# Kernel tuning notes

Hardware: AMD Instinct MI355X
Metric: run time of the kernel (lower is better)

The kernel has to match this reference:

```python
import jax, jax.numpy as jnp
import numpy as np

EPS = 1e-7  # tf.keras.backend.epsilon()
NUM_ROUTING = 3


def squash(v, axis=-1):
    s2 = jnp.sum(jnp.square(v), axis=axis, keepdims=True)
    scale = s2 / (1.0 + s2)
    return scale * v / jnp.sqrt(s2 + EPS)


def setup_inputs() -> dict:
    key = jax.random.key(0)
    kx, kw = jax.random.split(key)
    B, IN_CAPS, IN_DIM = 64, 2048, 16
    NUM_CAPS, OUT_DIM = 32, 16  # OUT_DIM must equal IN_DIM per the tf.matmul in call()
    x = jax.random.normal(kx, (B, IN_CAPS, IN_DIM), dtype=jnp.float32)
    # glorot_uniform over [in_caps, num_caps, in_dim, out_dim]
    limit = float(np.sqrt(6.0 / (IN_DIM + OUT_DIM)))
    W = jax.random.uniform(kw, (IN_CAPS, NUM_CAPS, IN_DIM, OUT_DIM),
                           minval=-limit, maxval=limit, dtype=jnp.float32)
    return {"x": x, "W": W}


def reference(x, W):
    # u_hat[b,i,j,d] = sum_k W[i,j,d,k] * x[b,i,k]   (tf.matmul(W, x[...,None]))
    u_hat = jnp.einsum('ijdk,bik->bijd', W, x)  # [B, in_caps, num_caps, dim]
    b = jnp.zeros(u_hat.shape[:-1], dtype=u_hat.dtype)  # [B, in_caps, num_caps]
    outputs = None
    for i in range(NUM_ROUTING):
        c = jax.nn.softmax(b, axis=2)                       # over num_caps
        s = jnp.einsum('bij,bijd->bjd', c, u_hat)           # weighted sum over in_caps
        outputs = squash(s)                                 # [B, num_caps, dim]
        if i < NUM_ROUTING - 1:
            b = b + jnp.einsum('bijd,bjd->bij', u_hat, outputs)  # agreement
    return outputs
```

## Files before the change

kernel.cpp:

```cpp
#include <hip/hip_runtime.h>
#include <cstdio>


#define B_TOT 64
#define IC    2048
#define KD    16
#define NC    32
#define OD    16
#define JD    512
#define NIC   256
#define IPB   (IC/NIC)
#define EPS_SQ 1e-7f

typedef __attribute__((ext_vector_type(4)))  short s16x4;
typedef __attribute__((ext_vector_type(8)))  short s16x8;
typedef __attribute__((ext_vector_type(16))) float f32x16;

__device__ inline short bfc(float f) {
  unsigned u = __builtin_bit_cast(unsigned, f);
  unsigned r = (u + 0x7FFFu + ((u >> 16) & 1u)) >> 16;
  return (short)(unsigned short)r;
}

__device__ inline f32x16 fz16() {
  f32x16 z;
#pragma unroll
  for (int q = 0; q < 16; q++) z[q] = 0.f;
  return z;
}

__global__ __launch_bounds__(256) void k_prep(const float* __restrict__ x,
                                              unsigned short* __restrict__ xp) {
  int t = blockIdx.x * 256 + threadIdx.x;
  int l  = t & 63;
  int bg = (t >> 6) & 1;
  int i  = t >> 7;
  int b  = bg * 32 + (l & 31);
  int hi = l >> 5;
  const float* s = x + ((size_t)b * IC + i) * KD + 4 * hi;
  float4 v0 = *(const float4*)(s);
  float4 v1 = *(const float4*)(s + 8);
  s16x8 r;
  r[0] = bfc(v0.x); r[1] = bfc(v0.y); r[2] = bfc(v0.z); r[3] = bfc(v0.w);
  r[4] = bfc(v1.x); r[5] = bfc(v1.y); r[6] = bfc(v1.z); r[7] = bfc(v1.w);
  *(s16x8*)(xp + (size_t)t * 8) = r;
}

template <bool FIRST>
__global__ __launch_bounds__(256, 2) void k_pass(const float* __restrict__ W,
                                                 const unsigned short* __restrict__ xp,
                                                 const float* __restrict__ ST,
                                                 _Float16* __restrict__ part) {
  __shared__ float lg[32][33];
  const int bid = blockIdx.x;
  const int bg  = bid & 1;
  const int ic  = bid >> 1;
  const int tid = threadIdx.x;
  const int w   = tid >> 6;
  const int l   = tid & 63;
  const int col = l & 31;
  const int hi  = l >> 5;

  f32x16 sa[4];
#pragma unroll
  for (int m = 0; m < 4; m++) sa[m] = fz16();

  float Sv[4][16];
  if (!FIRST) {
#pragma unroll
    for (int m = 0; m < 4; m++) {
      int mt = w * 4 + m;
#pragma unroll
      for (int r = 0; r < 16; r++) {
        int row = (r & 3) + 8 * (r >> 2) + 4 * hi;
        Sv[m][r] = ST[(size_t)(mt * 32 + row) * 64 + bg * 32 + col];
      }
    }
  }

  for (int ii = 0; ii < IPB; ii++) {
    int i = ic * IPB + ii;
    s16x8 xv  = *(const s16x8*)(xp + ((size_t)i * 2 + bg) * 512 + (size_t)l * 8);
    s16x4 xlo = __builtin_shufflevector(xv, xv, 0, 1, 2, 3);
    s16x4 xhi = __builtin_shufflevector(xv, xv, 4, 5, 6, 7);

    f32x16 D[4];
#pragma unroll
    for (int m = 0; m < 4; m++) {
      int mt = w * 4 + m;
      int jd = mt * 32 + col;
      const float* wp = W + ((size_t)i * JD + jd) * KD + 4 * hi;
      float4 a0 = *(const float4*)(wp);
      float4 a1 = *(const float4*)(wp + 8);
      s16x4 w0; w0[0]=bfc(a0.x); w0[1]=bfc(a0.y); w0[2]=bfc(a0.z); w0[3]=bfc(a0.w);
      s16x4 w1; w1[0]=bfc(a1.x); w1[1]=bfc(a1.y); w1[2]=bfc(a1.z); w1[3]=bfc(a1.w);
      f32x16 acc = FIRST ? sa[m] : fz16();
      acc = __builtin_amdgcn_mfma_f32_32x32x8bf16_1k(w0, xlo, acc, 0, 0, 0);
      acc = __builtin_amdgcn_mfma_f32_32x32x8bf16_1k(w1, xhi, acc, 0, 0, 0);
      if (FIRST) sa[m] = acc; else D[m] = acc;
    }

    if (!FIRST) {
#pragma unroll
      for (int m = 0; m < 4; m++) {
        float pe = 0.f, po = 0.f;
#pragma unroll
        for (int r = 0; r < 8; r++)  pe += D[m][r] * Sv[m][r];
#pragma unroll
        for (int r = 8; r < 16; r++) po += D[m][r] * Sv[m][r];
        pe += __shfl_xor(pe, 32);
        po += __shfl_xor(po, 32);
        int mt = w * 4 + m;
        if (l < 32) { lg[2 * mt][col] = pe; lg[2 * mt + 1][col] = po; }
      }
      __syncthreads();
      {
        int bb = w * 8 + (l >> 3);
        int sub = l & 7;
        float v0 = lg[sub * 4 + 0][bb], v1 = lg[sub * 4 + 1][bb];
        float v2 = lg[sub * 4 + 2][bb], v3 = lg[sub * 4 + 3][bb];
        float mx = fmaxf(fmaxf(v0, v1), fmaxf(v2, v3));
        mx = fmaxf(mx, __shfl_xor(mx, 1));
        mx = fmaxf(mx, __shfl_xor(mx, 2));
        mx = fmaxf(mx, __shfl_xor(mx, 4));
        v0 = __expf(v0 - mx); v1 = __expf(v1 - mx);
        v2 = __expf(v2 - mx); v3 = __expf(v3 - mx);
        float sm = v0 + v1 + v2 + v3;
        sm += __shfl_xor(sm, 1);
        sm += __shfl_xor(sm, 2);
        sm += __shfl_xor(sm, 4);
        float iv = 1.0f / sm;
        lg[sub * 4 + 0][bb] = v0 * iv; lg[sub * 4 + 1][bb] = v1 * iv;
        lg[sub * 4 + 2][bb] = v2 * iv; lg[sub * 4 + 3][bb] = v3 * iv;
      }
      __syncthreads();
#pragma unroll
      for (int m = 0; m < 4; m++) {
        int mt = w * 4 + m;
        float ce = lg[2 * mt][col];
        float co = lg[2 * mt + 1][col];
#pragma unroll
        for (int r = 0; r < 8; r++)  sa[m][r] += ce * D[m][r];
#pragma unroll
        for (int r = 8; r < 16; r++) sa[m][r] += co * D[m][r];
      }
      __syncthreads();
    }
  }

  const float sc = FIRST ? (1.0f / 32.0f) : 1.0f;
#pragma unroll
  for (int m = 0; m < 4; m++) {
    int mt = w * 4 + m;
#pragma unroll
    for (int r = 0; r < 16; r++) {
      int row = (r & 3) + 8 * (r >> 2) + 4 * hi;
      int jd = mt * 32 + row;
      part[(((size_t)bg * JD + jd) * NIC + ic) * 32 + col] = (_Float16)(sa[m][r] * sc);
    }
  }
}

template <bool FIRST, bool FINAL>
__global__ __launch_bounds__(512) void k_squash(const _Float16* __restrict__ part,
                                                float* __restrict__ ST,
                                                float* __restrict__ out) {
  __shared__ float sl[16][33];
  int bid = blockIdx.x;
  int bg = bid & 1, j = bid >> 1;
  int t = threadIdx.x;
  int b = t & 31, d = t >> 5;
  int jd = j * 16 + d;
  const _Float16* p = part + (((size_t)bg * JD + jd) * NIC) * 32 + b;
  float a0 = 0.f, a1 = 0.f, a2 = 0.f, a3 = 0.f;
  for (int q = 0; q < NIC; q += 4) {
    a0 += (float)p[(size_t)(q + 0) * 32];
    a1 += (float)p[(size_t)(q + 1) * 32];
    a2 += (float)p[(size_t)(q + 2) * 32];
    a3 += (float)p[(size_t)(q + 3) * 32];
  }
  float s = (a0 + a1) + (a2 + a3);
  sl[d][b] = s * s;
  __syncthreads();
  float s2 = 0.f;
#pragma unroll
  for (int dd = 0; dd < 16; dd++) s2 += sl[dd][b];
  float o = s * s2 / ((1.0f + s2) * sqrtf(s2 + EPS_SQ));
  if (FINAL) {
    out[((size_t)(bg * 32 + b) * NC + j) * OD + d] = o;
  } else if (FIRST) {
    ST[(size_t)jd * 64 + bg * 32 + b] = o;
  } else {
    ST[(size_t)jd * 64 + bg * 32 + b] += o;
  }
}

extern "C" void kernel_launch(void* const* d_in, const int* in_sizes, int n_in,
                              void* d_out, int out_size, void* d_ws, size_t ws_size,
                              hipStream_t stream) {
  (void)in_sizes; (void)n_in; (void)out_size;
  const float* x = (const float*)d_in[0];
  const float* W = (const float*)d_in[1];
  float* out = (float*)d_out;

  const size_t off_xp = 0;
  const size_t off_st = (size_t)4 << 20;
  const size_t off_pt = off_st + ((size_t)256 << 10);
  const size_t need = off_pt + (size_t)2 * JD * NIC * 32 * sizeof(_Float16) + 1024;
  fprintf(stderr, "[caps] ws_size=%zu need=%zu\n", ws_size, need);
  if (ws_size < need) return;

  unsigned short* xp = (unsigned short*)((char*)d_ws + off_xp);
  float*          ST = (float*)((char*)d_ws + off_st);
  _Float16*     part = (_Float16*)((char*)d_ws + off_pt);

  k_prep<<<dim3(1024), dim3(256), 0, stream>>>(x, xp);

  k_pass<true><<<dim3(512), dim3(256), 0, stream>>>(W, xp, ST, part);
  k_squash<true, false><<<dim3(64), dim3(512), 0, stream>>>(part, ST, out);
  k_pass<false><<<dim3(512), dim3(256), 0, stream>>>(W, xp, ST, part);
  k_squash<false, false><<<dim3(64), dim3(512), 0, stream>>>(part, ST, out);
  k_pass<false><<<dim3(512), dim3(256), 0, stream>>>(W, xp, ST, part);
  k_squash<false, true><<<dim3(64), dim3(512), 0, stream>>>(part, ST, out);
}
```

Measured before the change: 217.3 us.

## Prepack W to bf16 MFMA layout and split partial reduction into parallel stage

Adds a pre-pass that converts W once to bf16 in the exact per-lane MFMA fragment order, so each routing pass reads half the bytes with one 16-byte load per tile instead of converting fp32 three times. The cross-block sum over partials moves from 64 serial squash blocks into a 512-block reduction kernel followed by a small squash, raising parallelism. Routing coefficients ST are held as bf16 in registers to cut register pressure. The packed path needs an extra 32MB of workspace and falls back to the old path otherwise, and it adds kernel launches plus some precision loss in the agreement dot product.

```diff
diff --git a/kernel.cpp b/kernel.cpp
--- a/kernel.cpp
+++ b/kernel.cpp
@@ -2,9 +2,7 @@
 #include <cstdio>
 
 
-#define B_TOT 64
 #define IC    2048
-#define KD    16
 #define NC    32
 #define OD    16
 #define JD    512
@@ -12,16 +10,18 @@
 #define IPB   (IC/NIC)
 #define EPS_SQ 1e-7f
 
-typedef __attribute__((ext_vector_type(4)))  short s16x4;
-typedef __attribute__((ext_vector_type(8)))  short s16x8;
-typedef __attribute__((ext_vector_type(16))) float f32x16;
+typedef short  s16x4  __attribute__((ext_vector_type(4)));
+typedef short  s16x8  __attribute__((ext_vector_type(8)));
+typedef float  f32x16 __attribute__((ext_vector_type(16)));
 
 __device__ inline short bfc(float f) {
   unsigned u = __builtin_bit_cast(unsigned, f);
   unsigned r = (u + 0x7FFFu + ((u >> 16) & 1u)) >> 16;
   return (short)(unsigned short)r;
 }
-
+__device__ inline float bf2f(short s) {
+  return __builtin_bit_cast(float, ((unsigned)(unsigned short)s) << 16);
+}
 __device__ inline f32x16 fz16() {
   f32x16 z;
 #pragma unroll
@@ -29,15 +29,15 @@
   return z;
 }
 
-__global__ __launch_bounds__(256) void k_prep(const float* __restrict__ x,
-                                              unsigned short* __restrict__ xp) {
+__global__ __launch_bounds__(256) void k_prep_x(const float* __restrict__ x,
+                                                unsigned short* __restrict__ xp) {
   int t = blockIdx.x * 256 + threadIdx.x;
   int l  = t & 63;
   int bg = (t >> 6) & 1;
   int i  = t >> 7;
   int b  = bg * 32 + (l & 31);
   int hi = l >> 5;
-  const float* s = x + ((size_t)b * IC + i) * KD + 4 * hi;
+  const float* s = x + ((size_t)b * IC + i) * 16 + 4 * hi;
   float4 v0 = *(const float4*)(s);
   float4 v1 = *(const float4*)(s + 8);
   s16x8 r;
@@ -46,8 +46,44 @@
   *(s16x8*)(xp + (size_t)t * 8) = r;
 }
 
-template <bool FIRST>
+__global__ __launch_bounds__(256) void k_prep_w(const float* __restrict__ W,
+                                                unsigned short* __restrict__ wp) {
+  __shared__ unsigned lds[512 * 9];
+  const int i = blockIdx.x;
+  const int t = threadIdx.x;
+  const float* src = W + (size_t)i * 8192;
+#pragma unroll
+  for (int q = 0; q < 8; q++) {
+    int idx = q * 256 + t;
+    float4 v = *(const float4*)(src + (size_t)idx * 4);
+    unsigned p0 = ((unsigned)(unsigned short)bfc(v.x)) |
+                  (((unsigned)(unsigned short)bfc(v.y)) << 16);
+    unsigned p1 = ((unsigned)(unsigned short)bfc(v.z)) |
+                  (((unsigned)(unsigned short)bfc(v.w)) << 16);
+    int jd = idx >> 2;
+    int slot = (idx & 3) * 2;
+    lds[jd * 9 + slot]     = p0;
+    lds[jd * 9 + slot + 1] = p1;
+  }
+  __syncthreads();
+#pragma unroll
+  for (int q = 0; q < 4; q++) {
+    int f = q * 256 + t;
+    int mt = f >> 6, l = f & 63;
+    int col = l & 31, hi = l >> 5;
+    int jd = mt * 32 + col;
+    unsigned r0 = lds[jd * 9 + 2 * hi];
+    unsigned r1 = lds[jd * 9 + 2 * hi + 1];
+    unsigned r2 = lds[jd * 9 + 2 * hi + 4];
+    unsigned r3 = lds[jd * 9 + 2 * hi + 5];
+    uint4 o; o.x = r0; o.y = r1; o.z = r2; o.w = r3;
+    *(uint4*)(wp + ((size_t)i * 1024 + f) * 8) = o;
+  }
+}
+
+template <bool FIRST, bool PACKED>
 __global__ __launch_bounds__(256, 2) void k_pass(const float* __restrict__ W,
+                                                 const unsigned short* __restrict__ Wp,
                                                  const unsigned short* __restrict__ xp,
                                                  const float* __restrict__ ST,
                                                  _Float16* __restrict__ part) {
@@ -65,7 +101,7 @@
 #pragma unroll
   for (int m = 0; m < 4; m++) sa[m] = fz16();
 
-  float Sv[4][16];
+  s16x8 svA[4], svB[4];
   if (!FIRST) {
 #pragma unroll
     for (int m = 0; m < 4; m++) {
@@ -73,30 +109,46 @@
 #pragma unroll
       for (int r = 0; r < 16; r++) {
         int row = (r & 3) + 8 * (r >> 2) + 4 * hi;
-        Sv[m][r] = ST[(size_t)(mt * 32 + row) * 64 + bg * 32 + col];
+        float v = ST[(size_t)(mt * 32 + row) * 64 + bg * 32 + col];
+        short h = bfc(v);
+        if (r < 8) svA[m][r] = h; else svB[m][r - 8] = h;
       }
     }
   }
 
   for (int ii = 0; ii < IPB; ii++) {
     int i = ic * IPB + ii;
-    s16x8 xv  = *(const s16x8*)(xp + ((size_t)i * 2 + bg) * 512 + (size_t)l * 8);
+    s16x8 xv = *(const s16x8*)(xp + ((size_t)i * 2 + bg) * 512 + (size_t)l * 8);
     s16x4 xlo = __builtin_shufflevector(xv, xv, 0, 1, 2, 3);
     s16x4 xhi = __builtin_shufflevector(xv, xv, 4, 5, 6, 7);
 
+    s16x4 wlo[4], whi[4];
+    if (PACKED) {
+#pragma unroll
+      for (int m = 0; m < 4; m++) {
+        s16x8 wv = *(const s16x8*)(Wp + ((size_t)i * 1024 + (w * 4 + m) * 64 + l) * 8);
+        wlo[m] = __builtin_shufflevector(wv, wv, 0, 1, 2, 3);
+        whi[m] = __builtin_shufflevector(wv, wv, 4, 5, 6, 7);
+      }
+    } else {
+#pragma unroll
+      for (int m = 0; m < 4; m++) {
+        int jd = (w * 4 + m) * 32 + col;
+        const float* wq = W + ((size_t)i * JD + jd) * 16 + 4 * hi;
+        float4 a0 = *(const float4*)(wq);
+        float4 a1 = *(const float4*)(wq + 8);
+        s16x4 t0; t0[0]=bfc(a0.x); t0[1]=bfc(a0.y); t0[2]=bfc(a0.z); t0[3]=bfc(a0.w);
+        s16x4 t1; t1[0]=bfc(a1.x); t1[1]=bfc(a1.y); t1[2]=bfc(a1.z); t1[3]=bfc(a1.w);
+        wlo[m] = t0; whi[m] = t1;
+      }
+    }
+
     f32x16 D[4];
 #pragma unroll
     for (int m = 0; m < 4; m++) {
-      int mt = w * 4 + m;
-      int jd = mt * 32 + col;
-      const float* wp = W + ((size_t)i * JD + jd) * KD + 4 * hi;
-      float4 a0 = *(const float4*)(wp);
-      float4 a1 = *(const float4*)(wp + 8);
-      s16x4 w0; w0[0]=bfc(a0.x); w0[1]=bfc(a0.y); w0[2]=bfc(a0.z); w0[3]=bfc(a0.w);
-      s16x4 w1; w1[0]=bfc(a1.x); w1[1]=bfc(a1.y); w1[2]=bfc(a1.z); w1[3]=bfc(a1.w);
       f32x16 acc = FIRST ? sa[m] : fz16();
-      acc = __builtin_amdgcn_mfma_f32_32x32x8bf16_1k(w0, xlo, acc, 0, 0, 0);
-      acc = __builtin_amdgcn_mfma_f32_32x32x8bf16_1k(w1, xhi, acc, 0, 0, 0);
+      acc = __builtin_amdgcn_mfma_f32_32x32x8bf16_1k(wlo[m], xlo, acc, 0, 0, 0);
+      acc = __builtin_amdgcn_mfma_f32_32x32x8bf16_1k(whi[m], xhi, acc, 0, 0, 0);
       if (FIRST) sa[m] = acc; else D[m] = acc;
     }
 
@@ -105,9 +157,9 @@
       for (int m = 0; m < 4; m++) {
         float pe = 0.f, po = 0.f;
 #pragma unroll
-        for (int r = 0; r < 8; r++)  pe += D[m][r] * Sv[m][r];
-#pragma unroll
-        for (int r = 8; r < 16; r++) po += D[m][r] * Sv[m][r];
+        for (int r = 0; r < 8; r++)  pe += D[m][r]     * bf2f(svA[m][r]);
+#pragma unroll
+        for (int r = 0; r < 8; r++)  po += D[m][r + 8] * bf2f(svB[m][r]);
         pe += __shfl_xor(pe, 32);
         po += __shfl_xor(po, 32);
         int mt = w * 4 + m;
@@ -140,9 +192,9 @@
         float ce = lg[2 * mt][col];
         float co = lg[2 * mt + 1][col];
 #pragma unroll
-        for (int r = 0; r < 8; r++)  sa[m][r] += ce * D[m][r];
-#pragma unroll
-        for (int r = 8; r < 16; r++) sa[m][r] += co * D[m][r];
+        for (int r = 0; r < 8; r++)  sa[m][r]     += ce * D[m][r];
+#pragma unroll
+        for (int r = 0; r < 8; r++)  sa[m][r + 8] += co * D[m][r + 8];
       }
       __syncthreads();
     }
@@ -161,31 +213,44 @@
   }
 }
 
+__global__ __launch_bounds__(512) void k_red(const _Float16* __restrict__ part,
+                                             float* __restrict__ red) {
+  int bid = blockIdx.x;
+  int bg = bid & 1, j = (bid >> 1) & 31, q = bid >> 6;
+  int t = threadIdx.x;
+  int b = t & 31, d = t >> 5;
+  int jd = j * 16 + d;
+  const _Float16* p = part + (((size_t)(bg * JD + jd) * NIC) + q * 32) * 32 + b;
+  float a0 = 0.f, a1 = 0.f, a2 = 0.f, a3 = 0.f;
+#pragma unroll
+  for (int qq = 0; qq < 32; qq += 4) {
+    a0 += (float)p[(size_t)(qq + 0) * 32];
+    a1 += (float)p[(size_t)(qq + 1) * 32];
+    a2 += (float)p[(size_t)(qq + 2) * 32];
+    a3 += (float)p[(size_t)(qq + 3) * 32];
+  }
+  red[((size_t)(bg * 32 + j) * 8 + q) * 512 + t] = (a0 + a1) + (a2 + a3);
+}
+
 template <bool FIRST, bool FINAL>
-__global__ __launch_bounds__(512) void k_squash(const _Float16* __restrict__ part,
-                                                float* __restrict__ ST,
-                                                float* __restrict__ out) {
+__global__ __launch_bounds__(512) void k_squash2(const float* __restrict__ red,
+                                                 float* __restrict__ ST,
+                                                 float* __restrict__ out) {
   __shared__ float sl[16][33];
   int bid = blockIdx.x;
   int bg = bid & 1, j = bid >> 1;
   int t = threadIdx.x;
   int b = t & 31, d = t >> 5;
-  int jd = j * 16 + d;
-  const _Float16* p = part + (((size_t)bg * JD + jd) * NIC) * 32 + b;
-  float a0 = 0.f, a1 = 0.f, a2 = 0.f, a3 = 0.f;
-  for (int q = 0; q < NIC; q += 4) {
-    a0 += (float)p[(size_t)(q + 0) * 32];
-    a1 += (float)p[(size_t)(q + 1) * 32];
-    a2 += (float)p[(size_t)(q + 2) * 32];
-    a3 += (float)p[(size_t)(q + 3) * 32];
-  }
-  float s = (a0 + a1) + (a2 + a3);
+  float s = 0.f;
+#pragma unroll
+  for (int q = 0; q < 8; q++) s += red[((size_t)(bg * 32 + j) * 8 + q) * 512 + t];
   sl[d][b] = s * s;
   __syncthreads();
   float s2 = 0.f;
 #pragma unroll
   for (int dd = 0; dd < 16; dd++) s2 += sl[dd][b];
   float o = s * s2 / ((1.0f + s2) * sqrtf(s2 + EPS_SQ));
+  int jd = j * 16 + d;
   if (FINAL) {
     out[((size_t)(bg * 32 + b) * NC + j) * OD + d] = o;
   } else if (FIRST) {
@@ -203,23 +268,45 @@
   const float* W = (const float*)d_in[1];
   float* out = (float*)d_out;
 
-  const size_t off_xp = 0;
-  const size_t off_st = (size_t)4 << 20;
-  const size_t off_pt = off_st + ((size_t)256 << 10);
-  const size_t need = off_pt + (size_t)2 * JD * NIC * 32 * sizeof(_Float16) + 1024;
-  fprintf(stderr, "[caps] ws_size=%zu need=%zu\n", ws_size, need);
-  if (ws_size < need) return;
+  const size_t off_xp  = 0;
+  const size_t off_st  = (size_t)4 << 20;
+  const size_t off_red = off_st + ((size_t)256 << 10);
+  const size_t off_pt  = off_red + ((size_t)1 << 20);
+  const size_t off_wp  = off_pt + (size_t)2 * JD * NIC * 32 * sizeof(_Float16);
+  const size_t need_base = off_wp + 1024;
+  const size_t need_full = off_wp + (size_t)IC * 1024 * 16 + 1024;
+  fprintf(stderr, "[caps] ws_size=%zu need_base=%zu need_full=%zu\n",
+          ws_size, need_base, need_full);
+  if (ws_size < need_base) return;
+  const bool packed = (ws_size >= need_full);
 
   unsigned short* xp = (unsigned short*)((char*)d_ws + off_xp);
   float*          ST = (float*)((char*)d_ws + off_st);
+  float*         red = (float*)((char*)d_ws + off_red);
   _Float16*     part = (_Float16*)((char*)d_ws + off_pt);
-
-  k_prep<<<dim3(1024), dim3(256), 0, stream>>>(x, xp);
-
-  k_pass<true><<<dim3(512), dim3(256), 0, stream>>>(W, xp, ST, part);
-  k_squash<true, false><<<dim3(64), dim3(512), 0, stream>>>(part, ST, out);
-  k_pass<false><<<dim3(512), dim3(256), 0, stream>>>(W, xp, ST, part);
-  k_squash<false, false><<<dim3(64), dim3(512), 0, stream>>>(part, ST, out);
-  k_pass<false><<<dim3(512), dim3(256), 0, stream>>>(W, xp, ST, part);
-  k_squash<false, true><<<dim3(64), dim3(512), 0, stream>>>(part, ST, out);
-}
+  unsigned short* Wp = (unsigned short*)((char*)d_ws + off_wp);
+
+  k_prep_x<<<dim3(1024), dim3(256), 0, stream>>>(x, xp);
+  if (packed) {
+    k_prep_w<<<dim3(2048), dim3(256), 0, stream>>>(W, Wp);
+    k_pass<true, true><<<dim3(512), dim3(256), 0, stream>>>(W, Wp, xp, ST, part);
+  } else {
+    k_pass<true, false><<<dim3(512), dim3(256), 0, stream>>>(W, Wp, xp, ST, part);
+  }
+  k_red<<<dim3(512), dim3(512), 0, stream>>>(part, red);
+  k_squash2<true, false><<<dim3(64), dim3(512), 0, stream>>>(red, ST, out);
+
+  for (int pass = 1; pass < 3; pass++) {
+    if (packed) {
+      k_pass<false, true><<<dim3(512), dim3(256), 0, stream>>>(W, Wp, xp, ST, part);
+    } else {
+      k_pass<false, false><<<dim3(512), dim3(256), 0, stream>>>(W, Wp, xp, ST, part);
+    }
+    k_red<<<dim3(512), dim3(512), 0, stream>>>(part, red);
+    if (pass == 1) {
+      k_squash2<false, false><<<dim3(64), dim3(512), 0, stream>>>(red, ST, out);
+    } else {
+      k_squash2<false, true><<<dim3(64), dim3(512), 0, stream>>>(red, ST, out);
+    }
+  }
+}
```

New measurement: 190.2 us. -12.5%, faster.
